# Kernel tuning notes

Hardware: AMD Instinct MI355X
Metric: run time of the kernel (lower is better)

Reference implementation:

```python
import jax, jax.numpy as jnp
import numpy as np

B, S, D, H = 4, 2048, 1024, 16
HS = D // H  # head_size = 64


def setup_inputs() -> dict:
    key = jax.random.key(0)
    ks = jax.random.split(key, 6)
    scale = 1.0 / np.sqrt(D)
    return {
        "x": jax.random.normal(ks[0], (B, S, D), dtype=jnp.float32),
        "Wk": jax.random.normal(ks[1], (D, D), dtype=jnp.float32) * scale,
        "Wq": jax.random.normal(ks[2], (D, D), dtype=jnp.float32) * scale,
        "Wv": jax.random.normal(ks[3], (D, D), dtype=jnp.float32) * scale,
        "Wo": jax.random.normal(ks[4], (D, D), dtype=jnp.float32) * scale,
        "bo": jnp.zeros((D,), dtype=jnp.float32),
    }


def reference(x, Wk, Wq, Wv, Wo, bo):
    b, s, d = x.shape
    # torch nn.Linear: y = x @ W.T
    def heads(W):
        return (x @ W.T).reshape(b, s, H, HS).transpose(0, 2, 1, 3)  # [b,h,s,hs]
    k, q, v = heads(Wk), heads(Wq), heads(Wv)
    att = jnp.einsum("bhqd,bhkd->bhqk", q, k) * (1.0 / np.sqrt(HS))
    causal = jnp.tril(jnp.ones((s, s), dtype=bool))
    att = jnp.where(causal, att, -jnp.inf)
    att = jax.nn.softmax(att, axis=-1)
    # dropout in eval mode (identity) for deterministic reference
    out = jnp.einsum("bhqk,bhkd->bhqd", att, v)  # [b,h,s,hs]
    out = out.transpose(0, 2, 1, 3).reshape(b, s, d)
    return out @ Wo.T + bo
```

## Files before the change

kernel.cpp:

```cpp
#include <hip/hip_runtime.h>

#define B_ 4
#define S_ 2048
#define D_ 1024
#define H_ 16
#define HS_ 64

typedef float f32x4 __attribute__((ext_vector_type(4)));
typedef short bf16x8 __attribute__((ext_vector_type(8)));

__device__ inline short f2bf(float f) {
  union { float f; unsigned u; } v; v.f = f;
  unsigned r = v.u + 0x7fffu + ((v.u >> 16) & 1u);
  return (short)(r >> 16);
}
__device__ inline unsigned fbits(float f) {
  union { float f; unsigned u; } v; v.f = f; return v.u;
}

__device__ inline void load_lds16(const short* g, short* l) {
  __builtin_amdgcn_global_load_lds((const __attribute__((address_space(1))) void*)g,
                                   (__attribute__((address_space(3))) void*)l, 16, 0, 0);
}

__global__ __launch_bounds__(256) void cvt_f32_bf16(const float* __restrict__ in,
                                                    short* __restrict__ out, int n) {
  const int i = (blockIdx.x * 256 + threadIdx.x) * 4;
  if (i < n) {
    const float4 v = *(const float4*)(in + i);
    short4 o;
    o.x = f2bf(v.x); o.y = f2bf(v.y); o.z = f2bf(v.z); o.w = f2bf(v.w);
    *(short4*)(out + i) = o;
  }
}

__global__ __launch_bounds__(256) void cvt4_f32_bf16(const float* __restrict__ w0, const float* __restrict__ w1,
                                                     const float* __restrict__ w2, const float* __restrict__ w3,
                                                     short* __restrict__ o0, short* __restrict__ o1,
                                                     short* __restrict__ o2, short* __restrict__ o3, int n) {
  const float* in; short* out;
  switch (blockIdx.y) {
    case 0: in = w0; out = o0; break;
    case 1: in = w1; out = o1; break;
    case 2: in = w2; out = o2; break;
    default: in = w3; out = o3; break;
  }
  const int i = (blockIdx.x * 256 + threadIdx.x) * 4;
  if (i < n) {
    const float4 v = *(const float4*)(in + i);
    short4 o;
    o.x = f2bf(v.x); o.y = f2bf(v.y); o.z = f2bf(v.z); o.w = f2bf(v.w);
    *(short4*)(out + i) = o;
  }
}

__device__ inline void stage_tile64(const short* __restrict__ g, int ld, int k0,
                                    short* l, int tid) {
  const int srow = tid >> 3;
  const int scol = (tid & 7) * 8;
  const int scg  = ((tid & 7) ^ ((tid >> 3) & 7)) * 8;
  for (int j = 0; j < 4; j++)
    load_lds16(&g[(size_t)(srow + j * 32) * ld + k0 + scg], &l[(srow + j * 32) * 64 + scol]);
}

__device__ inline void mfma_core64(const short* lA, const short* lB, int wm, int wn,
                                   int col, int quad, f32x4 acc[4][4]) {
  for (int ks = 0; ks < 2; ks++) {
    const int cs = ((ks * 4 + quad) ^ (col & 7)) * 8;
    bf16x8 af[4], bfr[4];
    for (int i = 0; i < 4; i++) af[i]  = *(const bf16x8*)&lA[(wm + i * 16 + col) * 64 + cs];
    for (int j = 0; j < 4; j++) bfr[j] = *(const bf16x8*)&lB[(wn + j * 16 + col) * 64 + cs];
    for (int i = 0; i < 4; i++)
      for (int j = 0; j < 4; j++)
        acc[i][j] = __builtin_amdgcn_mfma_f32_16x16x32_bf16(af[i], bfr[j], acc[i][j], 0, 0, 0);
  }
}

template <bool CF32>
__global__ __launch_bounds__(256) void gemm_bb(const short* __restrict__ A,
                                               const short* __restrict__ Bt,
                                               void* __restrict__ Cv,
                                               const float* __restrict__ bias,
                                               int M, int N, int K) {
  __shared__ __align__(16) short lA[2][128 * 64];
  __shared__ __align__(16) short lB[2][128 * 64];
  const int tid = threadIdx.x;
  const int wave = tid >> 6, lane = tid & 63;
  const int quad = lane >> 4, col = lane & 15;
  const int m0 = blockIdx.x * 128, n0 = blockIdx.y * 128;
  const int wm = (wave >> 1) * 64, wn = (wave & 1) * 64;

  f32x4 acc[4][4];
  for (int i = 0; i < 4; i++)
    for (int j = 0; j < 4; j++) acc[i][j] = (f32x4){0.f, 0.f, 0.f, 0.f};

  const int NT = K >> 6;
  stage_tile64(&A[(size_t)m0 * K], K, 0, lA[0], tid);
  stage_tile64(&Bt[(size_t)n0 * K], K, 0, lB[0], tid);
  __syncthreads();
  for (int kt = 0; kt < NT; kt++) {
    const int cur = kt & 1;
    if (kt + 1 < NT) {
      stage_tile64(&A[(size_t)m0 * K], K, (kt + 1) * 64, lA[cur ^ 1], tid);
      stage_tile64(&Bt[(size_t)n0 * K], K, (kt + 1) * 64, lB[cur ^ 1], tid);
    }
    mfma_core64(lA[cur], lB[cur], wm, wn, col, quad, acc);
    __syncthreads();
  }

  for (int j = 0; j < 4; j++) {
    const int gn = n0 + wn + j * 16 + col;
    const float bv = bias ? bias[gn] : 0.f;
    for (int i = 0; i < 4; i++) {
      const int gm = m0 + wm + i * 16 + quad * 4;
      for (int r = 0; r < 4; r++) {
        if (CF32) ((float*)Cv)[(size_t)(gm + r) * N + gn] = acc[i][j][r] + bv;
        else      ((short*)Cv)[(size_t)(gm + r) * N + gn] = f2bf(acc[i][j][r] + bv);
      }
    }
  }
}

__global__ __launch_bounds__(256) void gemm_qkv(const short* __restrict__ A,
                                                const short* Wq, const short* Wk, const short* Wv,
                                                short* Cq, short* Ck, short* Cvt) {
  __shared__ __align__(16) short lA[2][128 * 64];
  __shared__ __align__(16) short lB[2][128 * 64];
  const int nsel = blockIdx.y >> 3;
  const int n0 = (blockIdx.y & 7) * 128;
  const short* Bt = nsel == 0 ? Wq : (nsel == 1 ? Wk : Wv);
  const int tid = threadIdx.x;
  const int wave = tid >> 6, lane = tid & 63;
  const int quad = lane >> 4, col = lane & 15;
  const int m0 = blockIdx.x * 128;
  const int wm = (wave >> 1) * 64, wn = (wave & 1) * 64;
  const int K = D_, N = D_;

  f32x4 acc[4][4];
  for (int i = 0; i < 4; i++)
    for (int j = 0; j < 4; j++) acc[i][j] = (f32x4){0.f, 0.f, 0.f, 0.f};

  const int NT = K >> 6;
  stage_tile64(&A[(size_t)m0 * K], K, 0, lA[0], tid);
  stage_tile64(&Bt[(size_t)n0 * K], K, 0, lB[0], tid);
  __syncthreads();
  for (int kt = 0; kt < NT; kt++) {
    const int cur = kt & 1;
    if (kt + 1 < NT) {
      stage_tile64(&A[(size_t)m0 * K], K, (kt + 1) * 64, lA[cur ^ 1], tid);
      stage_tile64(&Bt[(size_t)n0 * K], K, (kt + 1) * 64, lB[cur ^ 1], tid);
    }
    mfma_core64(lA[cur], lB[cur], wm, wn, col, quad, acc);
    __syncthreads();
  }

  if (nsel < 2) {
    short* C = nsel ? Ck : Cq;
    const float sc = nsel == 0 ? 0.18033688f : 1.0f;
    for (int j = 0; j < 4; j++) {
      const int gn = n0 + wn + j * 16 + col;
      for (int i = 0; i < 4; i++) {
        const int gm = m0 + wm + i * 16 + quad * 4;
        for (int r = 0; r < 4; r++)
          C[(size_t)(gm + r) * N + gn] = f2bf(acc[i][j][r] * sc);
      }
    }
  } else {
    for (int j = 0; j < 4; j++) {
      const int gn = n0 + wn + j * 16 + col;
      for (int i = 0; i < 4; i++) {
        const int gm = m0 + wm + i * 16 + quad * 4;
        const int bb = gm >> 11, s = gm & 2047;
        short4 o;
        o.x = f2bf(acc[i][j][0]); o.y = f2bf(acc[i][j][1]);
        o.z = f2bf(acc[i][j][2]); o.w = f2bf(acc[i][j][3]);
        *(short4*)&Cvt[((size_t)bb * D_ + gn) * (size_t)S_ + s] = o;
      }
    }
  }
}

__global__ __launch_bounds__(256) void flash_attn6(const short* __restrict__ Q,
                                                   const short* __restrict__ Kt,
                                                   const short* __restrict__ Vt,
                                                   short* __restrict__ O) {
  __shared__ __align__(16) short lK[2][64 * 64];
  __shared__ __align__(16) short lV[2][64 * 64];
  __shared__ __align__(16) short pl[4][16 * 64];
  const int tid = threadIdx.x, wave = tid >> 6, lane = tid & 63;
  const int quad = lane >> 4, col = lane & 15;
  const int bh = blockIdx.x;
  const int b = bh >> 4, h = bh & 15;
  const size_t qkbase = (size_t)b * S_ * D_ + (size_t)h * HS_;
  const size_t vtbase = ((size_t)b * D_ + (size_t)h * HS_) * (size_t)S_;

  const int srow = tid >> 3;
  const int scg = (tid & 7) ^ (srow & 7);
  const int cs0 = (quad ^ (col & 7)) * 8;
  const int cs1 = ((quad + 4) ^ (col & 7)) * 8;
  short* plw = pl[wave];

  bf16x8 ones;
  for (int i = 0; i < 8; i++) ones[i] = (short)0x3F80;

  int nb = 0;

  for (int half = 0; half < 2; half++) {
    const int s = half ? (int)blockIdx.y : 31 - (int)blockIdx.y;
    const int qmin = s * 64 + wave * 16;
    const int L = s;

    load_lds16(&Kt[qkbase + (size_t)srow * D_ + scg * 8],        &lK[nb][tid * 8]);
    load_lds16(&Kt[qkbase + (size_t)(32 + srow) * D_ + scg * 8], &lK[nb][2048 + tid * 8]);
    load_lds16(&Vt[vtbase + (size_t)srow * S_ + scg * 8],        &lV[nb][tid * 8]);
    load_lds16(&Vt[vtbase + (size_t)(srow + 32) * S_ + scg * 8], &lV[nb][2048 + tid * 8]);
    const int cur0 = nb;
    nb ^= 1;

    bf16x8 qf[2];
    for (int x = 0; x < 2; x++)
      qf[x] = *(const bf16x8*)&Q[qkbase + (size_t)(qmin + col) * D_ + x * 32 + quad * 8];

    f32x4 oacc[4], lacc;
    for (int dt = 0; dt < 4; dt++) oacc[dt] = (f32x4){0.f, 0.f, 0.f, 0.f};
    lacc = (f32x4){0.f, 0.f, 0.f, 0.f};

    for (int nt = 0; nt <= L; nt++) {
      const int n0 = nt * 64;
      const int cur = cur0 ^ (nt & 1);
      __syncthreads();
      if (nt < L) {
        const int nn = n0 + 64;
        load_lds16(&Kt[qkbase + (size_t)(nn + srow) * D_ + scg * 8],      &lK[nb][tid * 8]);
        load_lds16(&Kt[qkbase + (size_t)(nn + 32 + srow) * D_ + scg * 8], &lK[nb][2048 + tid * 8]);
        load_lds16(&Vt[vtbase + (size_t)srow * S_ + nn + scg * 8],        &lV[nb][tid * 8]);
        load_lds16(&Vt[vtbase + (size_t)(srow + 32) * S_ + nn + scg * 8], &lV[nb][2048 + tid * 8]);
        nb ^= 1;
      }

      const short* lKc = lK[cur];
      const short* lVc = lV[cur];
      const bool needM = (nt == L);

      bf16x8 kf[4][2];
      for (int t = 0; t < 4; t++) {
        const int rb = (t * 16 + col) * 64;
        kf[t][0] = *(const bf16x8*)&lKc[rb + cs0];
        kf[t][1] = *(const bf16x8*)&lKc[rb + cs1];
      }

      const int qg = qmin + col;
      for (int t = 0; t < 4; t++) {
        f32x4 z = (f32x4){0.f, 0.f, 0.f, 0.f};
        __builtin_amdgcn_s_setprio(1);
        z = __builtin_amdgcn_mfma_f32_16x16x32_bf16(kf[t][0], qf[0], z, 0, 0, 0);
        z = __builtin_amdgcn_mfma_f32_16x16x32_bf16(kf[t][1], qf[1], z, 0, 0, 0);
        __builtin_amdgcn_s_setprio(0);
        float p0 = exp2f(z[0]);
        float p1 = exp2f(z[1]);
        float p2 = exp2f(z[2]);
        float p3 = exp2f(z[3]);
        if (needM) {
          const int kv = n0 + t * 16 + quad * 4;
          if (kv + 0 > qg) p0 = 0.f;
          if (kv + 1 > qg) p1 = 0.f;
          if (kv + 2 > qg) p2 = 0.f;
          if (kv + 3 > qg) p3 = 0.f;
        }
        unsigned d0 = __builtin_amdgcn_perm(fbits(p1), fbits(p0), 0x07060302u);
        unsigned d1 = __builtin_amdgcn_perm(fbits(p3), fbits(p2), 0x07060302u);
        const int cc = (2 * t + (quad >> 1)) ^ (col & 7);
        uint2 w; w.x = d0; w.y = d1;
        *(uint2*)&plw[col * 64 + cc * 8 + (quad & 1) * 4] = w;
      }

      for (int h2 = 0; h2 < 2; h2++) {
        const int cgo = ((h2 * 4 + quad) ^ (col & 7)) * 8;
        const bf16x8 pf = *(const bf16x8*)&plw[col * 64 + cgo];
        bf16x8 vf[4];
        for (int dt = 0; dt < 4; dt++)
          vf[dt] = *(const bf16x8*)&lVc[(dt * 16 + col) * 64 + cgo];
        __builtin_amdgcn_s_setprio(1);
        lacc = __builtin_amdgcn_mfma_f32_16x16x32_bf16(pf, ones, lacc, 0, 0, 0);
        for (int dt = 0; dt < 4; dt++)
          oacc[dt] = __builtin_amdgcn_mfma_f32_16x16x32_bf16(pf, vf[dt], oacc[dt], 0, 0, 0);
        __builtin_amdgcn_s_setprio(0);
      }
    }

    for (int r = 0; r < 4; r++) {
      const float inv = 1.f / lacc[r];
      const size_t row = qkbase + (size_t)(qmin + quad * 4 + r) * D_;
      for (int dt = 0; dt < 4; dt++)
        O[row + dt * 16 + col] = f2bf(oacc[dt][r] * inv);
    }
  }
}

__global__ __launch_bounds__(256) void gemm_ff(const float* __restrict__ A,
                                               const float* __restrict__ Bt,
                                               short* __restrict__ C,
                                               int M, int N, int K) {
  __shared__ __align__(16) short lA[128 * 32];
  __shared__ __align__(16) short lB[128 * 32];
  const int tid = threadIdx.x;
  const int wave = tid >> 6, lane = tid & 63;
  const int quad = lane >> 4, col = lane & 15;
  const int m0 = blockIdx.y * 128, n0 = blockIdx.x * 128;
  const int wm = (wave >> 1) * 64, wn = (wave & 1) * 64;
  const int srow2 = tid >> 1;
  const int sc = (tid & 1) * 16;

  f32x4 acc[4][4];
  for (int i = 0; i < 4; i++)
    for (int j = 0; j < 4; j++) acc[i][j] = (f32x4){0.f, 0.f, 0.f, 0.f};

  for (int k0 = 0; k0 < K; k0 += 32) {
    __syncthreads();
    {
      const float4* ga = (const float4*)&A[(size_t)(m0 + srow2) * K + k0 + sc];
      const float4 v0 = ga[0], v1 = ga[1], v2 = ga[2], v3 = ga[3];
      bf16x8 p0, p1;
      p0[0] = f2bf(v0.x); p0[1] = f2bf(v0.y); p0[2] = f2bf(v0.z); p0[3] = f2bf(v0.w);
      p0[4] = f2bf(v1.x); p0[5] = f2bf(v1.y); p0[6] = f2bf(v1.z); p0[7] = f2bf(v1.w);
      p1[0] = f2bf(v2.x); p1[1] = f2bf(v2.y); p1[2] = f2bf(v2.z); p1[3] = f2bf(v2.w);
      p1[4] = f2bf(v3.x); p1[5] = f2bf(v3.y); p1[6] = f2bf(v3.z); p1[7] = f2bf(v3.w);
      *(bf16x8*)&lA[srow2 * 32 + sc]     = p0;
      *(bf16x8*)&lA[srow2 * 32 + sc + 8] = p1;
    }
    {
      const float4* gb = (const float4*)&Bt[(size_t)(n0 + srow2) * K + k0 + sc];
      const float4 v0 = gb[0], v1 = gb[1], v2 = gb[2], v3 = gb[3];
      bf16x8 p0, p1;
      p0[0] = f2bf(v0.x); p0[1] = f2bf(v0.y); p0[2] = f2bf(v0.z); p0[3] = f2bf(v0.w);
      p0[4] = f2bf(v1.x); p0[5] = f2bf(v1.y); p0[6] = f2bf(v1.z); p0[7] = f2bf(v1.w);
      p1[0] = f2bf(v2.x); p1[1] = f2bf(v2.y); p1[2] = f2bf(v2.z); p1[3] = f2bf(v2.w);
      p1[4] = f2bf(v3.x); p1[5] = f2bf(v3.y); p1[6] = f2bf(v3.z); p1[7] = f2bf(v3.w);
      *(bf16x8*)&lB[srow2 * 32 + sc]     = p0;
      *(bf16x8*)&lB[srow2 * 32 + sc + 8] = p1;
    }
    __syncthreads();
    {
      bf16x8 af[4], bfr[4];
      for (int i = 0; i < 4; i++) af[i]  = *(const bf16x8*)&lA[(wm + i * 16 + col) * 32 + quad * 8];
      for (int j = 0; j < 4; j++) bfr[j] = *(const bf16x8*)&lB[(wn + j * 16 + col) * 32 + quad * 8];
      for (int i = 0; i < 4; i++)
        for (int j = 0; j < 4; j++)
          acc[i][j] = __builtin_amdgcn_mfma_f32_16x16x32_bf16(af[i], bfr[j], acc[i][j], 0, 0, 0);
    }
  }

  for (int j = 0; j < 4; j++) {
    const int gn = n0 + wn + j * 16 + col;
    for (int i = 0; i < 4; i++) {
      const int gm = m0 + wm + i * 16 + quad * 4;
      for (int r = 0; r < 4; r++)
        C[(size_t)(gm + r) * N + gn] = f2bf(acc[i][j][r]);
    }
  }
}

__global__ __launch_bounds__(256) void gemm_out_bf(const short* __restrict__ A,
                                                   const float* __restrict__ Bt,
                                                   float* __restrict__ C,
                                                   const float* __restrict__ bias,
                                                   int M, int N, int K) {
  __shared__ __align__(16) short lA[128 * 32];
  __shared__ __align__(16) short lB[128 * 32];
  const int tid = threadIdx.x;
  const int wave = tid >> 6, lane = tid & 63;
  const int quad = lane >> 4, col = lane & 15;
  const int m0 = blockIdx.y * 128, n0 = blockIdx.x * 128;
  const int wm = (wave >> 1) * 64, wn = (wave & 1) * 64;
  const int srow = wave * 32 + (lane >> 2);
  const int scol = (lane & 3) * 8;
  const int srow2 = tid >> 1;
  const int sc = (tid & 1) * 16;

  f32x4 acc[4][4];
  for (int i = 0; i < 4; i++)
    for (int j = 0; j < 4; j++) acc[i][j] = (f32x4){0.f, 0.f, 0.f, 0.f};

  for (int k0 = 0; k0 < K; k0 += 32) {
    __syncthreads();
    load_lds16(&A[(size_t)(m0 + srow) * K + k0 + scol],      &lA[srow * 32 + scol]);
    load_lds16(&A[(size_t)(m0 + srow + 16) * K + k0 + scol], &lA[(srow + 16) * 32 + scol]);
    {
      const float4* gb = (const float4*)&Bt[(size_t)(n0 + srow2) * K + k0 + sc];
      const float4 v0 = gb[0], v1 = gb[1], v2 = gb[2], v3 = gb[3];
      bf16x8 p0, p1;
      p0[0] = f2bf(v0.x); p0[1] = f2bf(v0.y); p0[2] = f2bf(v0.z); p0[3] = f2bf(v0.w);
      p0[4] = f2bf(v1.x); p0[5] = f2bf(v1.y); p0[6] = f2bf(v1.z); p0[7] = f2bf(v1.w);
      p1[0] = f2bf(v2.x); p1[1] = f2bf(v2.y); p1[2] = f2bf(v2.z); p1[3] = f2bf(v2.w);
      p1[4] = f2bf(v3.x); p1[5] = f2bf(v3.y); p1[6] = f2bf(v3.z); p1[7] = f2bf(v3.w);
      *(bf16x8*)&lB[srow2 * 32 + sc]     = p0;
      *(bf16x8*)&lB[srow2 * 32 + sc + 8] = p1;
    }
    __syncthreads();
    {
      bf16x8 af[4], bfr[4];
      for (int i = 0; i < 4; i++) af[i]  = *(const bf16x8*)&lA[(wm + i * 16 + col) * 32 + quad * 8];
      for (int j = 0; j < 4; j++) bfr[j] = *(const bf16x8*)&lB[(wn + j * 16 + col) * 32 + quad * 8];
      for (int i = 0; i < 4; i++)
        for (int j = 0; j < 4; j++)
          acc[i][j] = __builtin_amdgcn_mfma_f32_16x16x32_bf16(af[i], bfr[j], acc[i][j], 0, 0, 0);
    }
  }

  for (int j = 0; j < 4; j++) {
    const int gn = n0 + wn + j * 16 + col;
    const float bv = bias ? bias[gn] : 0.f;
    for (int i = 0; i < 4; i++) {
      const int gm = m0 + wm + i * 16 + quad * 4;
      for (int r = 0; r < 4; r++)
        C[(size_t)(gm + r) * N + gn] = acc[i][j][r] + bv;
    }
  }
}

__global__ __launch_bounds__(64) void flash_attn(const short* __restrict__ Q,
                                                 const short* __restrict__ K,
                                                 const short* __restrict__ V,
                                                 short* __restrict__ O) {
  __shared__ __align__(16) short pl[16 * 40];
  const int lane = threadIdx.x;
  const int quad = lane >> 4, col = lane & 15;
  const int blk = blockIdx.x;
  const int qt = blk & 127;
  const int bh = blk >> 7;
  const int b = bh >> 4, h = bh & 15;
  const int q0 = qt * 16;
  const size_t base = (size_t)b * S_ * D_ + (size_t)h * HS_;

  const bf16x8 qf0 = *(const bf16x8*)&Q[base + (size_t)(q0 + col) * D_ + quad * 8];
  const bf16x8 qf1 = *(const bf16x8*)&Q[base + (size_t)(q0 + col) * D_ + 32 + quad * 8];

  float mr[4], lr[4];
  f32x4 oacc[4];
  for (int r = 0; r < 4; r++) { mr[r] = -1e30f; lr[r] = 0.f; }
  for (int dt = 0; dt < 4; dt++) oacc[dt] = (f32x4){0.f, 0.f, 0.f, 0.f};

  const int ntiles = (q0 + 15) / 32 + 1;
  for (int nt = 0; nt < ntiles; nt++) {
    const int n0 = nt * 32;
    f32x4 s[2];
    s[0] = (f32x4){0.f, 0.f, 0.f, 0.f};
    s[1] = (f32x4){0.f, 0.f, 0.f, 0.f};
    for (int t = 0; t < 2; t++) {
      const short* kp = &K[base + (size_t)(n0 + t * 16 + col) * D_ + quad * 8];
      const bf16x8 kf0 = *(const bf16x8*)kp;
      const bf16x8 kf1 = *(const bf16x8*)(kp + 32);
      s[t] = __builtin_amdgcn_mfma_f32_16x16x32_bf16(qf0, kf0, s[t], 0, 0, 0);
      s[t] = __builtin_amdgcn_mfma_f32_16x16x32_bf16(qf1, kf1, s[t], 0, 0, 0);
    }
    for (int r = 0; r < 4; r++) {
      const int mg = q0 + quad * 4 + r;
      float s0 = s[0][r] * 0.125f; if (n0 + col > mg)      s0 = -1e30f;
      float s1 = s[1][r] * 0.125f; if (n0 + 16 + col > mg) s1 = -1e30f;
      float tm = fmaxf(s0, s1);
      for (int off = 1; off < 16; off <<= 1) tm = fmaxf(tm, __shfl_xor(tm, off));
      const float mnew = fmaxf(mr[r], tm);
      const float alpha = __expf(mr[r] - mnew);
      mr[r] = mnew;
      const float p0 = __expf(s0 - mnew);
      const float p1 = __expf(s1 - mnew);
      float ps = p0 + p1;
      for (int off = 1; off < 16; off <<= 1) ps += __shfl_xor(ps, off);
      lr[r] = lr[r] * alpha + ps;
      for (int dt = 0; dt < 4; dt++) oacc[dt][r] *= alpha;
      pl[(quad * 4 + r) * 40 + col]      = f2bf(p0);
      pl[(quad * 4 + r) * 40 + 16 + col] = f2bf(p1);
    }
    const bf16x8 pf = *(const bf16x8*)&pl[col * 40 + quad * 8];
    for (int dt = 0; dt < 4; dt++) {
      bf16x8 vf;
      const short* vp = &V[base + (size_t)(n0 + quad * 8) * D_ + dt * 16 + col];
      for (int j = 0; j < 8; j++) vf[j] = vp[(size_t)j * D_];
      oacc[dt] = __builtin_amdgcn_mfma_f32_16x16x32_bf16(pf, vf, oacc[dt], 0, 0, 0);
    }
  }

  for (int r = 0; r < 4; r++) {
    const float inv = 1.f / lr[r];
    const size_t row = base + (size_t)(q0 + quad * 4 + r) * D_;
    for (int dt = 0; dt < 4; dt++)
      O[row + dt * 16 + col] = f2bf(oacc[dt][r] * inv);
  }
}

extern "C" void kernel_launch(void* const* d_in, const int* in_sizes, int n_in,
                              void* d_out, int out_size, void* d_ws, size_t ws_size,
                              hipStream_t stream) {
  const float* x  = (const float*)d_in[0];
  const float* Wk = (const float*)d_in[1];
  const float* Wq = (const float*)d_in[2];
  const float* Wv = (const float*)d_in[3];
  const float* Wo = (const float*)d_in[4];
  const float* bo = (const float*)d_in[5];
  float* out = (float*)d_out;

  char* ws = (char*)d_ws;
  const size_t MiB = 1u << 20;
  const int M = B_ * S_, N = D_, K = D_;
  const int nx = M * D_, nw = D_ * D_;

  if (ws_size >= 88 * MiB) {
    short* xb    = (short*)(ws);
    short* wkb   = (short*)(ws + 16 * MiB);
    short* wqb   = (short*)(ws + 18 * MiB);
    short* wvb   = (short*)(ws + 20 * MiB);
    short* wob   = (short*)(ws + 22 * MiB);
    short* q_ws  = (short*)(ws + 24 * MiB);
    short* k_ws  = (short*)(ws + 40 * MiB);
    short* vt_ws = (short*)(ws + 56 * MiB);
    short* a_ws  = (short*)(ws + 72 * MiB);

    hipLaunchKernelGGL(cvt_f32_bf16, dim3(nx / 1024), dim3(256), 0, stream, x, xb, nx);
    hipLaunchKernelGGL(cvt4_f32_bf16, dim3(nw / 1024, 4), dim3(256), 0, stream,
                       Wq, Wk, Wv, Wo, wqb, wkb, wvb, wob, nw);
    hipLaunchKernelGGL(gemm_qkv, dim3(M / 128, 24), dim3(256), 0, stream,
                       xb, wqb, wkb, wvb, q_ws, k_ws, vt_ws);
    hipLaunchKernelGGL(flash_attn6, dim3(B_ * H_, 16), dim3(256), 0, stream,
                       q_ws, k_ws, vt_ws, a_ws);
    hipLaunchKernelGGL((gemm_bb<true>), dim3(M / 128, N / 128), dim3(256), 0, stream,
                       a_ws, wob, (void*)out, bo, M, N, K);
  } else if (ws_size >= 64 * MiB) {
    short* q_ws = (short*)(ws);
    short* k_ws = (short*)(ws + 16 * MiB);
    short* v_ws = (short*)(ws + 32 * MiB);
    short* a_ws = (short*)(ws + 48 * MiB);
    dim3 gg(N / 128, M / 128), gb(256);
    hipLaunchKernelGGL(gemm_ff, gg, gb, 0, stream, x, Wq, q_ws, M, N, K);
    hipLaunchKernelGGL(gemm_ff, gg, gb, 0, stream, x, Wk, k_ws, M, N, K);
    hipLaunchKernelGGL(gemm_ff, gg, gb, 0, stream, x, Wv, v_ws, M, N, K);
    hipLaunchKernelGGL(flash_attn, dim3(B_ * H_ * (S_ / 16)), dim3(64), 0, stream, q_ws, k_ws, v_ws, a_ws);
    hipLaunchKernelGGL(gemm_out_bf, gg, gb, 0, stream, a_ws, Wo, out, bo, M, N, K);
  } else {
    short* q_ws = (short*)(ws);
    short* k_ws = (short*)(ws + 4 * MiB);
    short* v_ws = (short*)(ws + 8 * MiB);
    short* a_ws = (short*)(ws + 12 * MiB);
    const int Mb = S_;
    dim3 gg(N / 128, Mb / 128), gb(256);
    for (int b = 0; b < B_; b++) {
      const float* xb = x + (size_t)b * S_ * D_;
      float* ob = out + (size_t)b * S_ * D_;
      hipLaunchKernelGGL(gemm_ff, gg, gb, 0, stream, xb, Wq, q_ws, Mb, N, K);
      hipLaunchKernelGGL(gemm_ff, gg, gb, 0, stream, xb, Wk, k_ws, Mb, N, K);
      hipLaunchKernelGGL(gemm_ff, gg, gb, 0, stream, xb, Wv, v_ws, Mb, N, K);
      hipLaunchKernelGGL(flash_attn, dim3(H_ * (S_ / 16)), dim3(64), 0, stream, q_ws, k_ws, v_ws, a_ws);
      hipLaunchKernelGGL(gemm_out_bf, gg, gb, 0, stream, a_ws, Wo, ob, bo, Mb, N, K);
    }
  }
}
```

Baseline: 267.4 us.

## Rewrite QKV GEMM with 256x256 tiles, 8 waves, and phased async pipeline

Result: faster. 256.9 us (-3.9%).

```diff
diff --git a/kernel.cpp b/kernel.cpp
--- a/kernel.cpp
+++ b/kernel.cpp
@@ -121,37 +121,102 @@
   }
 }
 
-__global__ __launch_bounds__(256) void gemm_qkv(const short* __restrict__ A,
-                                                const short* Wq, const short* Wk, const short* Wv,
-                                                short* Cq, short* Ck, short* Cvt) {
-  __shared__ __align__(16) short lA[2][128 * 64];
-  __shared__ __align__(16) short lB[2][128 * 64];
-  const int nsel = blockIdx.y >> 3;
-  const int n0 = (blockIdx.y & 7) * 128;
-  const short* Bt = nsel == 0 ? Wq : (nsel == 1 ? Wk : Wv);
+__global__ __launch_bounds__(512, 2) void gemm_qkv8(const short* __restrict__ A,
+                                                    const short* Wq, const short* Wk, const short* Wv,
+                                                    short* Cq, short* Ck, short* Cvt) {
+  __shared__ __align__(16) short lds[2][2][256 * 64];
   const int tid = threadIdx.x;
   const int wave = tid >> 6, lane = tid & 63;
   const int quad = lane >> 4, col = lane & 15;
-  const int m0 = blockIdx.x * 128;
-  const int wm = (wave >> 1) * 64, wn = (wave & 1) * 64;
-  const int K = D_, N = D_;
-
-  f32x4 acc[4][4];
-  for (int i = 0; i < 4; i++)
-    for (int j = 0; j < 4; j++) acc[i][j] = (f32x4){0.f, 0.f, 0.f, 0.f};
-
-  const int NT = K >> 6;
-  stage_tile64(&A[(size_t)m0 * K], K, 0, lA[0], tid);
-  stage_tile64(&Bt[(size_t)n0 * K], K, 0, lB[0], tid);
-  __syncthreads();
-  for (int kt = 0; kt < NT; kt++) {
-    const int cur = kt & 1;
-    if (kt + 1 < NT) {
-      stage_tile64(&A[(size_t)m0 * K], K, (kt + 1) * 64, lA[cur ^ 1], tid);
-      stage_tile64(&Bt[(size_t)n0 * K], K, (kt + 1) * 64, lB[cur ^ 1], tid);
-    }
-    mfma_core64(lA[cur], lB[cur], wm, wn, col, quad, acc);
-    __syncthreads();
+  const int nsel = blockIdx.y >> 2;
+  const int n0 = (blockIdx.y & 3) * 256;
+  const short* Bt = nsel == 0 ? Wq : (nsel == 1 ? Wk : Wv);
+  const int m0 = blockIdx.x * 256;
+  const int wm = (wave >> 2) * 128, wn = (wave & 3) * 64;
+  const int K = D_;
+  const int NT = 16;
+
+  const int srow_base = ((tid >> 3) & 31) + ((tid >> 8) << 7);
+  const int sc8 = tid & 7;
+  const short* gA = &A[(size_t)m0 * K];
+  const short* gB = &Bt[(size_t)n0 * K];
+
+  auto stageA = [&](int t, int p) {
+    const int row = p * 32 + srow_base;
+    load_lds16(&gA[(size_t)row * K + t * 64 + ((sc8 ^ (row & 7)) * 8)],
+               &lds[t & 1][0][row * 64 + sc8 * 8]);
+  };
+  auto stageB = [&](int t, int p) {
+    const int row = p * 32 + srow_base;
+    load_lds16(&gB[(size_t)row * K + t * 64 + ((sc8 ^ (row & 7)) * 8)],
+               &lds[t & 1][1][row * 64 + sc8 * 8]);
+  };
+
+  f32x4 acc[8][4];
+#pragma unroll
+  for (int f = 0; f < 8; f++)
+#pragma unroll
+    for (int j = 0; j < 4; j++) acc[f][j] = (f32x4){0.f, 0.f, 0.f, 0.f};
+
+  for (int p = 0; p < 4; p++) stageA(0, p);
+  for (int p = 0; p < 4; p++) stageB(0, p);
+  for (int p = 0; p < 4; p++) stageB(1, p);
+  for (int p = 0; p < 3; p++) stageA(1, p);
+  asm volatile("s_waitcnt vmcnt(7)" ::: "memory");
+  __builtin_amdgcn_sched_barrier(0);
+  __builtin_amdgcn_s_barrier();
+
+  bf16x8 bfr[4][2];
+  for (int t = 0; t < NT; t++) {
+    const short* la = lds[t & 1][0];
+    const short* lb = lds[t & 1][1];
+
+#define QKV_PHASE(P, STAGES, GATE)                                                     \
+    {                                                                                  \
+      bf16x8 af[2][2];                                                                 \
+      if (P == 0) {                                                                    \
+        _Pragma("unroll")                                                              \
+        for (int j = 0; j < 4; j++)                                                    \
+          _Pragma("unroll")                                                            \
+          for (int kk = 0; kk < 2; kk++)                                               \
+            bfr[j][kk] = *(const bf16x8*)&lb[(wn + j * 16 + col) * 64 +                \
+                                             (((kk * 4 + quad) ^ (col & 7)) * 8)];     \
+      }                                                                                \
+      _Pragma("unroll")                                                                \
+      for (int f = 0; f < 2; f++)                                                      \
+        _Pragma("unroll")                                                              \
+        for (int kk = 0; kk < 2; kk++)                                                 \
+          af[f][kk] = *(const bf16x8*)&la[(wm + (P * 2 + f) * 16 + col) * 64 +         \
+                                          (((kk * 4 + quad) ^ (col & 7)) * 8)];        \
+      STAGES                                                                           \
+      __builtin_amdgcn_sched_barrier(0);                                               \
+      __builtin_amdgcn_s_barrier();                                                    \
+      asm volatile("s_waitcnt lgkmcnt(0)" ::: "memory");                               \
+      __builtin_amdgcn_sched_barrier(0);                                               \
+      __builtin_amdgcn_s_setprio(1);                                                   \
+      _Pragma("unroll")                                                                \
+      for (int f = 0; f < 2; f++)                                                      \
+        _Pragma("unroll")                                                              \
+        for (int j = 0; j < 4; j++)                                                    \
+          _Pragma("unroll")                                                            \
+          for (int kk = 0; kk < 2; kk++)                                               \
+            acc[P * 2 + f][j] = __builtin_amdgcn_mfma_f32_16x16x32_bf16(               \
+                af[f][kk], bfr[j][kk], acc[P * 2 + f][j], 0, 0, 0);                    \
+      __builtin_amdgcn_s_setprio(0);                                                   \
+      GATE                                                                             \
+      __builtin_amdgcn_sched_barrier(0);                                               \
+      __builtin_amdgcn_s_barrier();                                                    \
+    }
+
+    QKV_PHASE(0, { if (t + 1 < NT) stageA(t + 1, 3); }, {})
+    QKV_PHASE(1, { if (t + 2 < NT) { stageB(t + 2, 0); stageB(t + 2, 1); } }, {})
+    QKV_PHASE(2, { if (t + 2 < NT) { stageB(t + 2, 2); stageB(t + 2, 3); } }, {})
+    QKV_PHASE(3, { if (t + 2 < NT) { stageA(t + 2, 0); stageA(t + 2, 1); stageA(t + 2, 2); } },
+              {
+                if (t + 2 < NT)      { asm volatile("s_waitcnt vmcnt(7)" ::: "memory"); }
+                else if (t + 1 < NT) { asm volatile("s_waitcnt vmcnt(0)" ::: "memory"); }
+              })
+#undef QKV_PHASE
   }
 
   if (nsel < 2) {
@@ -159,21 +224,21 @@
     const float sc = nsel == 0 ? 0.18033688f : 1.0f;
     for (int j = 0; j < 4; j++) {
       const int gn = n0 + wn + j * 16 + col;
-      for (int i = 0; i < 4; i++) {
-        const int gm = m0 + wm + i * 16 + quad * 4;
+      for (int f = 0; f < 8; f++) {
+        const int gm = m0 + wm + f * 16 + quad * 4;
         for (int r = 0; r < 4; r++)
-          C[(size_t)(gm + r) * N + gn] = f2bf(acc[i][j][r] * sc);
+          C[(size_t)(gm + r) * D_ + gn] = f2bf(acc[f][j][r] * sc);
       }
     }
   } else {
     for (int j = 0; j < 4; j++) {
       const int gn = n0 + wn + j * 16 + col;
-      for (int i = 0; i < 4; i++) {
-        const int gm = m0 + wm + i * 16 + quad * 4;
+      for (int f = 0; f < 8; f++) {
+        const int gm = m0 + wm + f * 16 + quad * 4;
         const int bb = gm >> 11, s = gm & 2047;
         short4 o;
-        o.x = f2bf(acc[i][j][0]); o.y = f2bf(acc[i][j][1]);
-        o.z = f2bf(acc[i][j][2]); o.w = f2bf(acc[i][j][3]);
+        o.x = f2bf(acc[f][j][0]); o.y = f2bf(acc[f][j][1]);
+        o.z = f2bf(acc[f][j][2]); o.w = f2bf(acc[f][j][3]);
         *(short4*)&Cvt[((size_t)bb * D_ + gn) * (size_t)S_ + s] = o;
       }
     }
@@ -518,7 +583,7 @@
     hipLaunchKernelGGL(cvt_f32_bf16, dim3(nx / 1024), dim3(256), 0, stream, x, xb, nx);
     hipLaunchKernelGGL(cvt4_f32_bf16, dim3(nw / 1024, 4), dim3(256), 0, stream,
                        Wq, Wk, Wv, Wo, wqb, wkb, wvb, wob, nw);
-    hipLaunchKernelGGL(gemm_qkv, dim3(M / 128, 24), dim3(256), 0, stream,
+    hipLaunchKernelGGL(gemm_qkv8, dim3(M / 256, 12), dim3(512), 0, stream,
                        xb, wqb, wkb, wvb, q_ws, k_ws, vt_ws);
     hipLaunchKernelGGL(flash_attn6, dim3(B_ * H_, 16), dim3(256), 0, stream,
                        q_ws, k_ws, vt_ws, a_ws);
```

## Rewrite QKV GEMM with 128x256 tiles, 8 waves, triple-buffered swizzled LDS pipeline

Applied to the files above, without the earlier changes.

New measurement: 250.5 us. 1.07x faster.

```diff
diff --git a/kernel.cpp b/kernel.cpp
--- a/kernel.cpp
+++ b/kernel.cpp
@@ -121,37 +121,116 @@
   }
 }
 
-__global__ __launch_bounds__(256) void gemm_qkv(const short* __restrict__ A,
-                                                const short* Wq, const short* Wk, const short* Wv,
-                                                short* Cq, short* Ck, short* Cvt) {
-  __shared__ __align__(16) short lA[2][128 * 64];
-  __shared__ __align__(16) short lB[2][128 * 64];
-  const int nsel = blockIdx.y >> 3;
-  const int n0 = (blockIdx.y & 7) * 128;
-  const short* Bt = nsel == 0 ? Wq : (nsel == 1 ? Wk : Wv);
+__global__ __launch_bounds__(512, 2) void gemm_qkv8(const short* __restrict__ A,
+                                                    const short* Wq, const short* Wk, const short* Wv,
+                                                    short* Cq, short* Ck, short* Cvt) {
+  __shared__ __align__(16) short lds[3][24576];
   const int tid = threadIdx.x;
   const int wave = tid >> 6, lane = tid & 63;
   const int quad = lane >> 4, col = lane & 15;
+  const int nsel = blockIdx.y >> 2;
+  const int n0 = (blockIdx.y & 3) * 256;
+  const short* Bt = nsel == 0 ? Wq : (nsel == 1 ? Wk : Wv);
   const int m0 = blockIdx.x * 128;
-  const int wm = (wave >> 1) * 64, wn = (wave & 1) * 64;
-  const int K = D_, N = D_;
+  const int wm = (wave >> 2) * 64, wn = (wave & 3) * 64;
+  const int K = D_;
+  const int NT = 16;
+
+  const int srow = tid >> 3;
+  const int sc8 = tid & 7;
+  const short* gA = &A[(size_t)m0 * K];
+  const short* gB = &Bt[(size_t)n0 * K];
+
+  auto stageA = [&](int t, int p) {
+    const int row = p * 64 + srow;
+    load_lds16(&gA[(size_t)row * K + t * 64 + ((sc8 ^ (row & 7)) * 8)],
+               &lds[t % 3][row * 64 + sc8 * 8]);
+  };
+  auto stageB = [&](int t, int p) {
+    const int row = p * 64 + srow;
+    load_lds16(&gB[(size_t)row * K + t * 64 + ((sc8 ^ (row & 7)) * 8)],
+               &lds[t % 3][8192 + row * 64 + sc8 * 8]);
+  };
 
   f32x4 acc[4][4];
+#pragma unroll
   for (int i = 0; i < 4; i++)
+#pragma unroll
     for (int j = 0; j < 4; j++) acc[i][j] = (f32x4){0.f, 0.f, 0.f, 0.f};
 
-  const int NT = K >> 6;
-  stage_tile64(&A[(size_t)m0 * K], K, 0, lA[0], tid);
-  stage_tile64(&Bt[(size_t)n0 * K], K, 0, lB[0], tid);
-  __syncthreads();
-  for (int kt = 0; kt < NT; kt++) {
-    const int cur = kt & 1;
-    if (kt + 1 < NT) {
-      stage_tile64(&A[(size_t)m0 * K], K, (kt + 1) * 64, lA[cur ^ 1], tid);
-      stage_tile64(&Bt[(size_t)n0 * K], K, (kt + 1) * 64, lB[cur ^ 1], tid);
-    }
-    mfma_core64(lA[cur], lB[cur], wm, wn, col, quad, acc);
-    __syncthreads();
+  stageA(0, 0); stageA(0, 1);
+  for (int p = 0; p < 4; p++) stageB(0, p);
+  stageA(1, 0); stageA(1, 1);
+  for (int p = 0; p < 4; p++) stageB(1, p);
+  asm volatile("s_waitcnt vmcnt(6)" ::: "memory");
+  __builtin_amdgcn_sched_barrier(0);
+  __builtin_amdgcn_s_barrier();
+
+  for (int t = 0; t < NT; t++) {
+    const short* la = lds[t % 3];
+    const short* lb = la + 8192;
+
+    bf16x8 bfr[4][2];
+    {
+      bf16x8 af[2][2];
+#pragma unroll
+      for (int j = 0; j < 4; j++)
+#pragma unroll
+        for (int kk = 0; kk < 2; kk++)
+          bfr[j][kk] = *(const bf16x8*)&lb[(wn + j * 16 + col) * 64 +
+                                           (((kk * 4 + quad) ^ (col & 7)) * 8)];
+#pragma unroll
+      for (int f = 0; f < 2; f++)
+#pragma unroll
+        for (int kk = 0; kk < 2; kk++)
+          af[f][kk] = *(const bf16x8*)&la[(wm + f * 16 + col) * 64 +
+                                          (((kk * 4 + quad) ^ (col & 7)) * 8)];
+      if (t + 2 < NT) { stageB(t + 2, 0); stageB(t + 2, 1); stageB(t + 2, 2); }
+      __builtin_amdgcn_sched_barrier(0);
+      __builtin_amdgcn_s_barrier();
+      asm volatile("s_waitcnt lgkmcnt(0)" ::: "memory");
+      __builtin_amdgcn_sched_barrier(0);
+      __builtin_amdgcn_s_setprio(1);
+#pragma unroll
+      for (int f = 0; f < 2; f++)
+#pragma unroll
+        for (int j = 0; j < 4; j++)
+#pragma unroll
+          for (int kk = 0; kk < 2; kk++)
+            acc[f][j] = __builtin_amdgcn_mfma_f32_16x16x32_bf16(
+                af[f][kk], bfr[j][kk], acc[f][j], 0, 0, 0);
+      __builtin_amdgcn_s_setprio(0);
+      __builtin_amdgcn_sched_barrier(0);
+      __builtin_amdgcn_s_barrier();
+    }
+    {
+      bf16x8 af[2][2];
+#pragma unroll
+      for (int f = 0; f < 2; f++)
+#pragma unroll
+        for (int kk = 0; kk < 2; kk++)
+          af[f][kk] = *(const bf16x8*)&la[(wm + (2 + f) * 16 + col) * 64 +
+                                          (((kk * 4 + quad) ^ (col & 7)) * 8)];
+      if (t + 2 < NT) { stageB(t + 2, 3); stageA(t + 2, 0); stageA(t + 2, 1); }
+      __builtin_amdgcn_sched_barrier(0);
+      __builtin_amdgcn_s_barrier();
+      asm volatile("s_waitcnt lgkmcnt(0)" ::: "memory");
+      __builtin_amdgcn_sched_barrier(0);
+      __builtin_amdgcn_s_setprio(1);
+#pragma unroll
+      for (int f = 0; f < 2; f++)
+#pragma unroll
+        for (int j = 0; j < 4; j++)
+#pragma unroll
+          for (int kk = 0; kk < 2; kk++)
+            acc[2 + f][j] = __builtin_amdgcn_mfma_f32_16x16x32_bf16(
+                af[f][kk], bfr[j][kk], acc[2 + f][j], 0, 0, 0);
+      __builtin_amdgcn_s_setprio(0);
+      if (t + 2 < NT)      { asm volatile("s_waitcnt vmcnt(6)" ::: "memory"); }
+      else if (t + 1 < NT) { asm volatile("s_waitcnt vmcnt(0)" ::: "memory"); }
+      __builtin_amdgcn_sched_barrier(0);
+      __builtin_amdgcn_s_barrier();
+    }
   }
 
   if (nsel < 2) {
@@ -162,7 +241,7 @@
       for (int i = 0; i < 4; i++) {
         const int gm = m0 + wm + i * 16 + quad * 4;
         for (int r = 0; r < 4; r++)
-          C[(size_t)(gm + r) * N + gn] = f2bf(acc[i][j][r] * sc);
+          C[(size_t)(gm + r) * D_ + gn] = f2bf(acc[i][j][r] * sc);
       }
     }
   } else {
@@ -518,7 +597,7 @@
     hipLaunchKernelGGL(cvt_f32_bf16, dim3(nx / 1024), dim3(256), 0, stream, x, xb, nx);
     hipLaunchKernelGGL(cvt4_f32_bf16, dim3(nw / 1024, 4), dim3(256), 0, stream,
                        Wq, Wk, Wv, Wo, wqb, wkb, wvb, wob, nw);
-    hipLaunchKernelGGL(gemm_qkv, dim3(M / 128, 24), dim3(256), 0, stream,
+    hipLaunchKernelGGL(gemm_qkv8, dim3(M / 128, 12), dim3(512), 0, stream,
                        xb, wqb, wkb, wvb, q_ws, k_ws, vt_ws);
     hipLaunchKernelGGL(flash_attn6, dim3(B_ * H_, 16), dim3(256), 0, stream,
                        q_ws, k_ws, vt_ws, a_ws);
```
